# Optimization experiments

Hardware: AMD Instinct MI355X
Metric: run time of the kernel (lower is better)

Reference implementation:

```python
import jax, jax.numpy as jnp
import numpy as np

N, D, H = 1024, 256, 256


def setup_inputs() -> dict:
    key = jax.random.key(0)
    k1, k2, k3, k4, k5 = jax.random.split(key, 5)
    z = jax.random.normal(k1, (N, D), dtype=jnp.float32)
    # fc1: Linear(2*D, H) -> weight [H, 2*D], bias [H]
    lim1 = 1.0 / np.sqrt(2 * D)
    W1 = jax.random.uniform(k2, (H, 2 * D), dtype=jnp.float32, minval=-lim1, maxval=lim1)
    b1 = jax.random.uniform(k3, (H,), dtype=jnp.float32, minval=-lim1, maxval=lim1)
    # fc2: Linear(H, 1)
    lim2 = 1.0 / np.sqrt(H)
    W2 = jax.random.uniform(k4, (1, H), dtype=jnp.float32, minval=-lim2, maxval=lim2)
    b2 = jax.random.uniform(k5, (1,), dtype=jnp.float32, minval=-lim2, maxval=lim2)
    return {"z": z, "W1": W1, "b1": b1, "W2": W2, "b2": b2}


def reference(z, W1, b1, W2, b2):
    # fc1 applied to concat([row, col]) splits algebraically:
    # cat(row, col) @ W1.T = row @ W1[:, :D].T + col @ W1[:, D:].T
    row_part = z @ W1[:, :D].T            # [N, H] (contribution of row element)
    col_part = z @ W1[:, D:].T            # [N, H] (contribution of col element)
    h = jax.nn.relu(row_part[:, None, :] + col_part[None, :, :] + b1)  # [N, N, H]
    out = jax.nn.sigmoid(jnp.einsum('ijh,h->ij', h, W2[0]) + b2[0])    # [N, N]
    return out
```

## Files before the change

kernel.cpp:

```cpp
#include <hip/hip_runtime.h>

#define NN 1024

typedef __attribute__((ext_vector_type(8))) short short8;
typedef __attribute__((ext_vector_type(4))) float floatx4;
typedef __attribute__((ext_vector_type(4))) unsigned int uint4v;
typedef _Float16 half2v __attribute__((ext_vector_type(2)));

#define R2_OFF   0u
#define CT_OFF   524288u

__device__ __forceinline__ unsigned short f2bf(float x) {
  unsigned u = __float_as_uint(x);
  return (unsigned short)((u + 0x7FFFu + ((u >> 16) & 1u)) >> 16);
}

__device__ __forceinline__ unsigned int pkf16(float a, float b) {
  unsigned int lo = (unsigned int)__builtin_bit_cast(unsigned short, (_Float16)a);
  unsigned int hi = (unsigned int)__builtin_bit_cast(unsigned short, (_Float16)b);
  return lo | (hi << 16);
}

__device__ __forceinline__ void dot2acc(unsigned int a, unsigned int b, float& acc) {
#if __has_builtin(__builtin_amdgcn_fdot2)
  acc = __builtin_amdgcn_fdot2(__builtin_bit_cast(half2v, a),
                               __builtin_bit_cast(half2v, b), acc, false);
#else
  asm("v_dot2_f32_f16 %0, %1, %2, %0" : "+v"(acc) : "v"(a), "v"(b));
#endif
}

__device__ __forceinline__ void pkmaxdot(unsigned int r, unsigned int c,
                                         unsigned int mul, float& acc) {
  unsigned int m;
  asm("v_pk_max_f16 %0, %1, %2" : "=v"(m) : "v"(r), "v"(c));
  dot2acc(m, mul, acc);
}

__global__ __launch_bounds__(256) void k1_fused(const float* __restrict__ z,
    const float* __restrict__ W1, const float* __restrict__ b1,
    const float* __restrict__ W2, char* __restrict__ ws) {
  __shared__ unsigned short zsh[16][272];
  __shared__ unsigned short wsh[4][16][272];
  __shared__ float tile[4][16][17];
  unsigned int* R2 = (unsigned int*)(ws + R2_OFF);
  unsigned int* Ct = (unsigned int*)(ws + CT_OFF);

  const int t = threadIdx.x;
  const int l = t & 63, w = t >> 6;
  const int i0 = blockIdx.x * 16;
  const int tid = blockIdx.y * 4 + w;
  const int q0 = tid * 16;
  const bool topR = q0 < 256;
  const int h0 = q0 & 255;
  const int off = topR ? 0 : 256;

  #pragma unroll
  for (int k = 0; k < 4; ++k) {
    const int f = t + k * 256;
    const int r = f >> 6, c4 = f & 63;
    const float4 v = *(const float4*)(z + (i0 + r) * 256 + c4 * 4);
    ushort4 u;
    u.x = f2bf(v.x); u.y = f2bf(v.y); u.z = f2bf(v.z); u.w = f2bf(v.w);
    *(ushort4*)&zsh[r][c4 * 4] = u;
  }
  #pragma unroll 4
  for (int r = 0; r < 16; ++r) {
    const int h = h0 + r;
    const float wa = fabsf(W2[h]);
    const float sc = topR ? wa : -wa;
    const float4 v = *(const float4*)(W1 + h * 512 + off + l * 4);
    ushort4 u;
    u.x = f2bf(v.x * sc); u.y = f2bf(v.y * sc);
    u.z = f2bf(v.z * sc); u.w = f2bf(v.w * sc);
    *(ushort4*)&wsh[w][r][l * 4] = u;
  }
  __syncthreads();

  floatx4 acc = {0.f, 0.f, 0.f, 0.f};
  const int fr = l & 15, fg = (l >> 4) * 8;
  #pragma unroll
  for (int kk = 0; kk < 8; ++kk) {
    const short8 a  = *(const short8*)&zsh[fr][fg + kk * 32];
    const short8 bb = *(const short8*)&wsh[w][fr][fg + kk * 32];
    acc = __builtin_amdgcn_mfma_f32_16x16x32_bf16(a, bb, acc, 0, 0, 0);
  }

  const int col = l & 15, r0 = (l >> 4) * 4;
  float bias = 0.f;
  if (topR) {
    const int h = q0 + col;
    bias = b1[h] * fabsf(W2[h]);
  }
  #pragma unroll
  for (int q = 0; q < 4; ++q) tile[w][r0 + q][col] = acc[q] + bias;
  __syncthreads();
  const int il = l & 15, g2 = l >> 4;
  if (topR) {
    #pragma unroll
    for (int e = 0; e < 2; ++e) {
      const int qc = g2 * 4 + e * 2;
      const unsigned int pk = pkf16(tile[w][il][qc], tile[w][il][qc + 1]);
      R2[((q0 >> 1) + g2 * 2 + e) * 1024 + (i0 + il)] = pk;
    }
  } else {
    const unsigned int pk0 = pkf16(tile[w][il][g2 * 4 + 0], tile[w][il][g2 * 4 + 1]);
    const unsigned int pk1 = pkf16(tile[w][il][g2 * 4 + 2], tile[w][il][g2 * 4 + 3]);
    const int hpg = ((q0 - 256) >> 3) + (g2 >> 1);
    unsigned int* dst = Ct + (hpg * 1024 + (i0 + il)) * 4 + (g2 & 1) * 2;
    dst[0] = pk0; dst[1] = pk1;
  }
}

__global__ __launch_bounds__(256) void k2_pair(const unsigned int* __restrict__ R2,
    const unsigned int* __restrict__ Ct, const float* __restrict__ W2,
    const float* __restrict__ b2v, float* __restrict__ out) {
  __shared__ unsigned int MulS[128];
  const int t = threadIdx.x;
  if (t < 128) {
    const unsigned int s0 = (W2[2 * t]     > 0.f) ? 0x3C00u : 0xBC00u;
    const unsigned int s1 = (W2[2 * t + 1] > 0.f) ? 0x3C00u : 0xBC00u;
    MulS[t] = s0 | (s1 << 16);
  }
  __syncthreads();

  const int lane = t & 63;
  const int w = __builtin_amdgcn_readfirstlane(t >> 6);
  const int i0 = blockIdx.x * 16 + w * 4;
  const int j  = blockIdx.y * 64 + lane;

  float acc0 = 0.f, acc1 = 0.f, acc2 = 0.f, acc3 = 0.f, kv = 0.f;

  #pragma unroll 4
  for (int g = 0; g < 32; ++g) {
    const uint4v cc = *(const uint4v*)(Ct + (g * 1024 + j) * 4);
    const uint4v mq = *(const uint4v*)&MulS[g * 4];
    #pragma unroll
    for (int p = 0; p < 4; ++p) {
      const uint4v ra = *(const uint4v*)(R2 + (g * 4 + p) * 1024 + i0);
      const unsigned int c = cc[p], mu = mq[p];
      dot2acc(c, mu, kv);
      pkmaxdot(ra[0], c, mu, acc0);
      pkmaxdot(ra[1], c, mu, acc1);
      pkmaxdot(ra[2], c, mu, acc2);
      pkmaxdot(ra[3], c, mu, acc3);
    }
  }

  const float base = b2v[0] - kv;
  out[(i0 + 0) * NN + j] = 1.f / (1.f + __expf(-(acc0 + base)));
  out[(i0 + 1) * NN + j] = 1.f / (1.f + __expf(-(acc1 + base)));
  out[(i0 + 2) * NN + j] = 1.f / (1.f + __expf(-(acc2 + base)));
  out[(i0 + 3) * NN + j] = 1.f / (1.f + __expf(-(acc3 + base)));
}

extern "C" void kernel_launch(void* const* d_in, const int* in_sizes, int n_in,
                              void* d_out, int out_size, void* d_ws, size_t ws_size,
                              hipStream_t stream) {
  const float* z  = (const float*)d_in[0];
  const float* W1 = (const float*)d_in[1];
  const float* b1 = (const float*)d_in[2];
  const float* W2 = (const float*)d_in[3];
  const float* b2 = (const float*)d_in[4];
  float* out = (float*)d_out;
  char* ws = (char*)d_ws;

  k1_fused<<<dim3(64, 8), 256, 0, stream>>>(z, W1, b1, W2, ws);
  k2_pair<<<dim3(64, 16), 256, 0, stream>>>(
      (const unsigned int*)(ws + R2_OFF), (const unsigned int*)(ws + CT_OFF),
      W2, b2, out);
}
```

Measured before the change: 26.37 us.

## Switch pair kernel to fp32 with LDS-staged row tiles and split-H reduction

```diff
diff --git a/kernel.cpp b/kernel.cpp
--- a/kernel.cpp
+++ b/kernel.cpp
@@ -4,37 +4,13 @@
 
 typedef __attribute__((ext_vector_type(8))) short short8;
 typedef __attribute__((ext_vector_type(4))) float floatx4;
-typedef __attribute__((ext_vector_type(4))) unsigned int uint4v;
-typedef _Float16 half2v __attribute__((ext_vector_type(2)));
 
-#define R2_OFF   0u
-#define CT_OFF   524288u
+#define RF_OFF   0u
+#define CF_OFF   1048576u
 
 __device__ __forceinline__ unsigned short f2bf(float x) {
   unsigned u = __float_as_uint(x);
   return (unsigned short)((u + 0x7FFFu + ((u >> 16) & 1u)) >> 16);
-}
-
-__device__ __forceinline__ unsigned int pkf16(float a, float b) {
-  unsigned int lo = (unsigned int)__builtin_bit_cast(unsigned short, (_Float16)a);
-  unsigned int hi = (unsigned int)__builtin_bit_cast(unsigned short, (_Float16)b);
-  return lo | (hi << 16);
-}
-
-__device__ __forceinline__ void dot2acc(unsigned int a, unsigned int b, float& acc) {
-#if __has_builtin(__builtin_amdgcn_fdot2)
-  acc = __builtin_amdgcn_fdot2(__builtin_bit_cast(half2v, a),
-                               __builtin_bit_cast(half2v, b), acc, false);
-#else
-  asm("v_dot2_f32_f16 %0, %1, %2, %0" : "+v"(acc) : "v"(a), "v"(b));
-#endif
-}
-
-__device__ __forceinline__ void pkmaxdot(unsigned int r, unsigned int c,
-                                         unsigned int mul, float& acc) {
-  unsigned int m;
-  asm("v_pk_max_f16 %0, %1, %2" : "=v"(m) : "v"(r), "v"(c));
-  dot2acc(m, mul, acc);
 }
 
 __global__ __launch_bounds__(256) void k1_fused(const float* __restrict__ z,
@@ -43,8 +19,8 @@
   __shared__ unsigned short zsh[16][272];
   __shared__ unsigned short wsh[4][16][272];
   __shared__ float tile[4][16][17];
-  unsigned int* R2 = (unsigned int*)(ws + R2_OFF);
-  unsigned int* Ct = (unsigned int*)(ws + CT_OFF);
+  float* Rf = (float*)(ws + RF_OFF);
+  float* Cf = (float*)(ws + CF_OFF);
 
   const int t = threadIdx.x;
   const int l = t & 63, w = t >> 6;
@@ -98,60 +74,96 @@
   const int il = l & 15, g2 = l >> 4;
   if (topR) {
     #pragma unroll
-    for (int e = 0; e < 2; ++e) {
-      const int qc = g2 * 4 + e * 2;
-      const unsigned int pk = pkf16(tile[w][il][qc], tile[w][il][qc + 1]);
-      R2[((q0 >> 1) + g2 * 2 + e) * 1024 + (i0 + il)] = pk;
+    for (int e = 0; e < 4; ++e) {
+      const int qc = g2 * 4 + e;
+      Rf[(q0 + qc) * 1024 + i0 + il] = tile[w][il][qc];
     }
   } else {
-    const unsigned int pk0 = pkf16(tile[w][il][g2 * 4 + 0], tile[w][il][g2 * 4 + 1]);
-    const unsigned int pk1 = pkf16(tile[w][il][g2 * 4 + 2], tile[w][il][g2 * 4 + 3]);
     const int hpg = ((q0 - 256) >> 3) + (g2 >> 1);
-    unsigned int* dst = Ct + (hpg * 1024 + (i0 + il)) * 4 + (g2 & 1) * 2;
-    dst[0] = pk0; dst[1] = pk1;
+    float4 v;
+    v.x = tile[w][il][g2 * 4 + 0]; v.y = tile[w][il][g2 * 4 + 1];
+    v.z = tile[w][il][g2 * 4 + 2]; v.w = tile[w][il][g2 * 4 + 3];
+    *(float4*)(Cf + (hpg * 1024 + (i0 + il)) * 8 + (g2 & 1) * 4) = v;
   }
 }
 
-__global__ __launch_bounds__(256) void k2_pair(const unsigned int* __restrict__ R2,
-    const unsigned int* __restrict__ Ct, const float* __restrict__ W2,
+__global__ __launch_bounds__(256) void k2_pair(const float* __restrict__ Rf,
+    const float* __restrict__ Cf, const float* __restrict__ W2,
     const float* __restrict__ b2v, float* __restrict__ out) {
-  __shared__ unsigned int MulS[128];
+  __shared__ float Rl[256][16];
+  __shared__ float part[4][16][65];
+  __shared__ float partkv[4][64];
+  __shared__ float MulS[256];
   const int t = threadIdx.x;
-  if (t < 128) {
-    const unsigned int s0 = (W2[2 * t]     > 0.f) ? 0x3C00u : 0xBC00u;
-    const unsigned int s1 = (W2[2 * t + 1] > 0.f) ? 0x3C00u : 0xBC00u;
-    MulS[t] = s0 | (s1 << 16);
+  const int lane = t & 63, w = t >> 6;
+  const int li = lane >> 4, lj = lane & 15;
+  const int i0 = blockIdx.x * 16, j0 = blockIdx.y * 64;
+
+  MulS[t] = (W2[t] > 0.f) ? 1.f : -1.f;
+  #pragma unroll
+  for (int k = 0; k < 4; ++k) {
+    const int f = t + k * 256;
+    const int h = f >> 2, c4 = f & 3;
+    *(float4*)&Rl[h][c4 * 4] = *(const float4*)(Rf + h * 1024 + i0 + c4 * 4);
   }
   __syncthreads();
 
-  const int lane = t & 63;
-  const int w = __builtin_amdgcn_readfirstlane(t >> 6);
-  const int i0 = blockIdx.x * 16 + w * 4;
-  const int j  = blockIdx.y * 64 + lane;
+  const int hbase = w * 8;
+  float acc[4][4] = {};
+  float kv[4] = {};
 
-  float acc0 = 0.f, acc1 = 0.f, acc2 = 0.f, acc3 = 0.f, kv = 0.f;
+  #pragma unroll 2
+  for (int g = 0; g < 8; ++g) {
+    const int hpg = hbase + g;
+    float carr[4][8];
+    #pragma unroll
+    for (int jj = 0; jj < 4; ++jj) {
+      const float* cp = Cf + (hpg * 1024 + j0 + lj + 16 * jj) * 8;
+      *(float4*)&carr[jj][0] = *(const float4*)cp;
+      *(float4*)&carr[jj][4] = *(const float4*)(cp + 4);
+    }
+    float sarr[8];
+    *(float4*)&sarr[0] = *(const float4*)&MulS[hpg * 8];
+    *(float4*)&sarr[4] = *(const float4*)&MulS[hpg * 8 + 4];
 
-  #pragma unroll 4
-  for (int g = 0; g < 32; ++g) {
-    const uint4v cc = *(const uint4v*)(Ct + (g * 1024 + j) * 4);
-    const uint4v mq = *(const uint4v*)&MulS[g * 4];
     #pragma unroll
-    for (int p = 0; p < 4; ++p) {
-      const uint4v ra = *(const uint4v*)(R2 + (g * 4 + p) * 1024 + i0);
-      const unsigned int c = cc[p], mu = mq[p];
-      dot2acc(c, mu, kv);
-      pkmaxdot(ra[0], c, mu, acc0);
-      pkmaxdot(ra[1], c, mu, acc1);
-      pkmaxdot(ra[2], c, mu, acc2);
-      pkmaxdot(ra[3], c, mu, acc3);
+    for (int e = 0; e < 8; ++e) {
+      const int h = hpg * 8 + e;
+      const float4 ra = *(const float4*)&Rl[h][li * 4];
+      const float sh = sarr[e];
+      #pragma unroll
+      for (int jj = 0; jj < 4; ++jj) {
+        const float c = carr[jj][e];
+        kv[jj] = fmaf(sh, c, kv[jj]);
+        acc[0][jj] = fmaf(fmaxf(ra.x, c), sh, acc[0][jj]);
+        acc[1][jj] = fmaf(fmaxf(ra.y, c), sh, acc[1][jj]);
+        acc[2][jj] = fmaf(fmaxf(ra.z, c), sh, acc[2][jj]);
+        acc[3][jj] = fmaf(fmaxf(ra.w, c), sh, acc[3][jj]);
+      }
     }
   }
 
-  const float base = b2v[0] - kv;
-  out[(i0 + 0) * NN + j] = 1.f / (1.f + __expf(-(acc0 + base)));
-  out[(i0 + 1) * NN + j] = 1.f / (1.f + __expf(-(acc1 + base)));
-  out[(i0 + 2) * NN + j] = 1.f / (1.f + __expf(-(acc2 + base)));
-  out[(i0 + 3) * NN + j] = 1.f / (1.f + __expf(-(acc3 + base)));
+  #pragma unroll
+  for (int ii = 0; ii < 4; ++ii)
+    #pragma unroll
+    for (int jj = 0; jj < 4; ++jj)
+      part[w][li * 4 + ii][lj + 16 * jj] = acc[ii][jj];
+  if (li == 0) {
+    #pragma unroll
+    for (int jj = 0; jj < 4; ++jj) partkv[w][lj + 16 * jj] = kv[jj];
+  }
+  __syncthreads();
+
+  const int jl = t & 63, ib = (t >> 6) * 4;
+  const float kvt = partkv[0][jl] + partkv[1][jl] + partkv[2][jl] + partkv[3][jl];
+  const float base = b2v[0] - kvt;
+  #pragma unroll
+  for (int u = 0; u < 4; ++u) {
+    const int il = ib + u;
+    const float x = part[0][il][jl] + part[1][il][jl] +
+                    part[2][il][jl] + part[3][il][jl] + base;
+    out[(i0 + il) * NN + j0 + jl] = 1.f / (1.f + __expf(-x));
+  }
 }
 
 extern "C" void kernel_launch(void* const* d_in, const int* in_sizes, int n_in,
@@ -167,6 +179,6 @@
 
   k1_fused<<<dim3(64, 8), 256, 0, stream>>>(z, W1, b1, W2, ws);
   k2_pair<<<dim3(64, 16), 256, 0, stream>>>(
-      (const unsigned int*)(ws + R2_OFF), (const unsigned int*)(ws + CT_OFF),
+      (const float*)(ws + RF_OFF), (const float*)(ws + CF_OFF),
       W2, b2, out);
 }
```

After: 33.24 us. 1.26x slower.
